# Performance work log

Measured on AMD Instinct MI355X. Metric: run time of the kernel, lower is better.

The kernel has to match this reference:

```python
import jax, jax.numpy as jnp
import numpy as np

N_NODES = 50000
N_EDGES = 800000
D_IN = 128
D_OUT = 128


def setup_inputs() -> dict:
    key = jax.random.key(0)
    k_feat, k_src, k_dst, k_ws, k_bs, k_wn = jax.random.split(key, 6)
    feat = jax.random.normal(k_feat, (N_NODES, D_IN), dtype=jnp.float32)
    src = jax.random.randint(k_src, (N_EDGES,), 0, N_NODES, dtype=jnp.int64)
    dst = jax.random.randint(k_dst, (N_EDGES,), 0, N_NODES, dtype=jnp.int64)
    # fc_self: Linear(D_IN, D_OUT, bias=True); fc_neigh: Linear(D_IN, D_OUT, bias=False)
    W_self = jax.random.normal(k_ws, (D_OUT, D_IN), dtype=jnp.float32) * (1.0 / np.sqrt(D_IN))
    b_self = jax.random.normal(k_bs, (D_OUT,), dtype=jnp.float32) * 0.01
    # xavier_uniform with relu gain
    gain = float(np.sqrt(2.0))
    bound = gain * float(np.sqrt(6.0 / (D_IN + D_OUT)))
    W_neigh = jax.random.uniform(k_wn, (D_OUT, D_IN), dtype=jnp.float32, minval=-bound, maxval=bound)
    bias = jnp.zeros((D_OUT,), dtype=jnp.float32)
    return {"feat": feat, "src": src, "dst": dst, "W_self": W_self,
            "b_self": b_self, "W_neigh": W_neigh, "bias": bias}


def reference(feat, src, dst, W_self, b_self, W_neigh, bias):
    # copy_u('h','m') + fn.mean('m','neigh'): gather src feats, mean-reduce by dst.
    # lin_before_mp is False (in_feats == out_feats), so aggregate raw feats first.
    n = feat.shape[0]
    msgs = feat[src]                                             # [E, D_IN]
    neigh_sum = jax.ops.segment_sum(msgs, dst, num_segments=n)   # [N, D_IN]
    deg = jax.ops.segment_sum(jnp.ones(src.shape, feat.dtype), dst, num_segments=n)
    # DGL mean yields 0 for zero-in-degree nodes
    h_neigh = jnp.where(deg[:, None] > 0, neigh_sum / jnp.maximum(deg, 1.0)[:, None], 0.0)
    h_neigh = h_neigh @ W_neigh.T                                # fc_neigh (no bias)
    h_self = feat @ W_self.T + b_self                            # fc_self
    return h_self + h_neigh + bias
```

## Files before the change

### kernel.cpp

```cpp
#include <hip/hip_runtime.h>
#include <hip/hip_fp8.h>

#define N_NODES 50000
#define N_EDGES 800000
#define D 128
#define NBUK 782
#define CAPB 1344
#define SRTN (CAPB + 64*7)
#define EPB 2048
#define SCAT_BLOCKS 391
#define FEAT_BLOCKS 3125
#define W_BLOCKS 32
#define CAPC 16

typedef __bf16 bf16x8 __attribute__((ext_vector_type(8)));
typedef __bf16 bf16x4 __attribute__((ext_vector_type(4)));
typedef float  f32x4  __attribute__((ext_vector_type(4)));
typedef float  f32x2  __attribute__((ext_vector_type(2)));

#if defined(__has_builtin)
#if __has_builtin(__builtin_amdgcn_cvt_pk_f32_fp8) && __has_builtin(__builtin_amdgcn_cvt_pk_fp8_f32)
#define HW_FP8 1
#endif
#endif

#define OFF_PACKED 0ull
#define OFF_FEAT8  19568768ull
#define OFF_WC16   25968896ull
#define OFF_BIASC  26034432ull
#define OFF_FEAT16 26035200ull

__device__ __forceinline__ float fp8tof_sw(unsigned char b) {
    __hip_fp8_e4m3 t; t.__x = b;
    return (float)t;
}

__global__ __launch_bounds__(256)
void prep_kernel(const int* __restrict__ src, const int* __restrict__ dst,
                 int* __restrict__ packed,
                 const float* __restrict__ feat, unsigned char* __restrict__ feat8,
                 __bf16* __restrict__ feat16,
                 const float* __restrict__ Ws, const float* __restrict__ Wn,
                 const float* __restrict__ b_self, const float* __restrict__ bias,
                 __bf16* __restrict__ Wc16, float* __restrict__ biasc, int n) {
    const int tid = threadIdx.x;
    const int bid = blockIdx.x;
    if (bid < SCAT_BLOCKS) {
        __shared__ int hist[NBUK];
        __shared__ int boff[NBUK];
        __shared__ int srtL[EPB];
        __shared__ int wtot[4];
        const int e0 = bid * EPB;
        int d[8], s[8];
        for (int i = tid; i < NBUK; i += 256) hist[i] = 0;
        __syncthreads();
        #pragma unroll
        for (int j = 0; j < 8; ++j) {
            int e = e0 + j * 256 + tid;
            bool ok = e < n;
            d[j] = ok ? dst[e] : -1;
            s[j] = ok ? src[e] : 0;
            if (ok) atomicAdd(&hist[d[j] >> 6], 1);
        }
        __syncthreads();
        {
            const int lane = tid & 63;
            const int wv = tid >> 6;
            const int b4 = tid * 4;
            int h0 = (b4 + 0 < NBUK) ? hist[b4 + 0] : 0;
            int h1 = (b4 + 1 < NBUK) ? hist[b4 + 1] : 0;
            int h2 = (b4 + 2 < NBUK) ? hist[b4 + 2] : 0;
            int h3 = (b4 + 3 < NBUK) ? hist[b4 + 3] : 0;
            int sm = h0 + h1 + h2 + h3;
            int v = sm;
            #pragma unroll
            for (int o = 1; o < 64; o <<= 1) {
                int u = __shfl_up(v, o);
                if (lane >= o) v += u;
            }
            if (lane == 63) wtot[wv] = v;
            __syncthreads();
            if (tid == 0) {
                int r = 0;
                #pragma unroll
                for (int j = 0; j < 4; ++j) { int t = wtot[j]; wtot[j] = r; r += t; }
            }
            __syncthreads();
            int ex = wtot[wv] + v - sm;
            if (b4 + 0 < NBUK) { boff[b4 + 0] = ex;                hist[b4 + 0] = 0; }
            if (b4 + 1 < NBUK) { boff[b4 + 1] = ex + h0;           hist[b4 + 1] = 0; }
            if (b4 + 2 < NBUK) { boff[b4 + 2] = ex + h0 + h1;      hist[b4 + 2] = 0; }
            if (b4 + 3 < NBUK) { boff[b4 + 3] = ex + h0 + h1 + h2; hist[b4 + 3] = 0; }
        }
        __syncthreads();
        #pragma unroll
        for (int j = 0; j < 8; ++j) {
            if (d[j] >= 0) {
                int bk = d[j] >> 6;
                int r = atomicAdd(&hist[bk], 1);
                srtL[boff[bk] + r] = ((d[j] & 63) << 16) | s[j];
            }
        }
        __syncthreads();
        for (int idx = tid; idx < NBUK * 4; idx += 256) {
            int bk = idx >> 2;
            int q4 = (idx & 3) * 4;
            int off = boff[bk];
            int c = hist[bk];
            int4 v;
            v.x = (q4 + 0 < c) ? srtL[off + q4 + 0] : -1;
            v.y = (q4 + 1 < c) ? srtL[off + q4 + 1] : -1;
            v.z = (q4 + 2 < c) ? srtL[off + q4 + 2] : -1;
            v.w = (q4 + 3 < c) ? srtL[off + q4 + 3] : -1;
            *(int4*)&packed[((size_t)bk * SCAT_BLOCKS + bid) * CAPC + q4] = v;
        }
    } else if (bid < SCAT_BLOCKS + FEAT_BLOCKS) {
        size_t i = ((size_t)(bid - SCAT_BLOCKS) * 256 + tid) * 8;
        float4 f0 = *(const float4*)(feat + i);
        float4 f1 = *(const float4*)(feat + i + 4);
        bf16x8 t16;
        t16[0]=(__bf16)f0.x; t16[1]=(__bf16)f0.y; t16[2]=(__bf16)f0.z; t16[3]=(__bf16)f0.w;
        t16[4]=(__bf16)f1.x; t16[5]=(__bf16)f1.y; t16[6]=(__bf16)f1.z; t16[7]=(__bf16)f1.w;
        *(bf16x8*)(feat16 + i) = t16;
#ifdef HW_FP8
        int q0 = __builtin_amdgcn_cvt_pk_fp8_f32(f0.x, f0.y, 0, false);
        q0     = __builtin_amdgcn_cvt_pk_fp8_f32(f0.z, f0.w, q0, true);
        int q1 = __builtin_amdgcn_cvt_pk_fp8_f32(f1.x, f1.y, 0, false);
        q1     = __builtin_amdgcn_cvt_pk_fp8_f32(f1.z, f1.w, q1, true);
        uint2 qq; qq.x = (unsigned)q0; qq.y = (unsigned)q1;
        *(uint2*)(feat8 + i) = qq;
#else
        float fv[8] = {f0.x, f0.y, f0.z, f0.w, f1.x, f1.y, f1.z, f1.w};
        union { unsigned char b[8]; unsigned long long u; } q;
        #pragma unroll
        for (int j = 0; j < 8; ++j) { __hip_fp8_e4m3 e(fv[j]); q.b[j] = e.__x; }
        *(unsigned long long*)(feat8 + i) = q.u;
#endif
    } else if (bid < SCAT_BLOCKS + FEAT_BLOCKS + W_BLOCKS) {
        int idx = (bid - SCAT_BLOCKS - FEAT_BLOCKS) * 256 + tid;
        int col = idx >> 6;
        int kq  = (idx & 63) * 4;
        const float* srcp = (kq < D) ? (Ws + (size_t)col * D + kq)
                                     : (Wn + (size_t)col * D + (kq - D));
        float4 f = *(const float4*)srcp;
        bf16x4 t;
        t[0]=(__bf16)f.x; t[1]=(__bf16)f.y; t[2]=(__bf16)f.z; t[3]=(__bf16)f.w;
        *(bf16x4*)(Wc16 + (size_t)col * 256 + kq) = t;
    } else {
        if (tid < D) biasc[tid] = b_self[tid] + bias[tid];
        else if (tid < D + 32)
            ((unsigned*)(feat8 + (size_t)N_NODES * D))[tid - 128] = 0u;
    }
}

__global__ __launch_bounds__(512)
void fused_kernel(const __bf16* __restrict__ feat16,
                  const unsigned char* __restrict__ feat8,
                  const int* __restrict__ packed,
                  const __bf16* __restrict__ Wc16,
                  const float* __restrict__ biasc,
                  float* __restrict__ out) {
    __shared__ __bf16 At[64][264];
    __shared__ unsigned short srt[SRTN];
    __shared__ int cnt[64];
    __shared__ int loff[64];
    __shared__ int degs[64];
    const int tid = threadIdx.x;
    const int b = blockIdx.x;
    const int node0 = b * 64;

    const int srow = tid >> 3;
    const int scol = (tid & 7) * 16;
    const int snn = node0 + srow;
    bf16x8 st0 = {}, st1 = {};
    if (snn < N_NODES) {
        const __bf16* sp = feat16 + (size_t)snn * D + scol;
        st0 = *(const bf16x8*)sp;
        st1 = *(const bf16x8*)(sp + 8);
    }

    if (tid < 64) cnt[tid] = 0;
    __syncthreads();

    int4 vv0, vv1, vv2, vv3;
    {
        const int4* sp = (const int4*)(packed + (size_t)b * SCAT_BLOCKS * CAPC);
        int4 none; none.x = -1; none.y = -1; none.z = -1; none.w = -1;
        int i0 = tid, i1 = 512 + tid, i2 = 1024 + tid, i3 = 1536 + tid;
        vv0 = sp[i0];
        vv1 = sp[i1];
        vv2 = (i2 < SCAT_BLOCKS * 4) ? sp[i2] : none;
        vv3 = (i3 < SCAT_BLOCKS * 4) ? sp[i3] : none;
        #define HISTV(v) do { \
            if ((v).x != -1) atomicAdd(&cnt[(v).x >> 16], 1); \
            if ((v).y != -1) atomicAdd(&cnt[(v).y >> 16], 1); \
            if ((v).z != -1) atomicAdd(&cnt[(v).z >> 16], 1); \
            if ((v).w != -1) atomicAdd(&cnt[(v).w >> 16], 1); } while (0)
        HISTV(vv0); HISTV(vv1); HISTV(vv2); HISTV(vv3);
        #undef HISTV
    }
    __syncthreads();

    if (tid < 64) {
        int c = cnt[tid];
        int cp = (c + 7) & ~7;
        int v = cp;
        #pragma unroll
        for (int o = 1; o < 64; o <<= 1) {
            int u = __shfl_up(v, o);
            if (tid >= o) v += u;
        }
        loff[tid] = v - cp;
        degs[tid] = c;
        cnt[tid] = 0;
    }
    __syncthreads();

    *(bf16x8*)&At[srow][scol] = st0;
    *(bf16x8*)&At[srow][scol + 8] = st1;
    {
        #define SCATV(v) do { \
            if ((v).x != -1) { int l = (v).x >> 16; int r = atomicAdd(&cnt[l], 1); int o = loff[l] + r; if (o < SRTN) srt[o] = (unsigned short)(v).x; } \
            if ((v).y != -1) { int l = (v).y >> 16; int r = atomicAdd(&cnt[l], 1); int o = loff[l] + r; if (o < SRTN) srt[o] = (unsigned short)(v).y; } \
            if ((v).z != -1) { int l = (v).z >> 16; int r = atomicAdd(&cnt[l], 1); int o = loff[l] + r; if (o < SRTN) srt[o] = (unsigned short)(v).z; } \
            if ((v).w != -1) { int l = (v).w >> 16; int r = atomicAdd(&cnt[l], 1); int o = loff[l] + r; if (o < SRTN) srt[o] = (unsigned short)(v).w; } } while (0)
        SCATV(vv0); SCATV(vv1); SCATV(vv2); SCATV(vv3);
        #undef SCATV
    }
    if (tid < 64) {
        int c = degs[tid];
        int cp = (c + 7) & ~7;
        int base0 = loff[tid];
        for (int j = c; j < cp; ++j)
            if (base0 + j < SRTN) srt[base0 + j] = (unsigned short)N_NODES;
    }
    __syncthreads();

    {
        const int hw = tid >> 5;
        const int lane = tid & 31;
        const unsigned int* g8 = (const unsigned int*)feat8;
        #pragma unroll
        for (int t = 0; t < 4; ++t) {
            int i = hw + t * 16;
            int dg = degs[i];
            int dgp = (dg + 7) & ~7;
            const int base0 = loff[i];
            float a0 = 0.f, a1 = 0.f, a2 = 0.f, a3 = 0.f;
            for (int j = 0; j < dgp; j += 8) {
                int s[8]; unsigned int w[8];
                #pragma unroll
                for (int q = 0; q < 8; ++q) s[q] = srt[base0 + j + q];
                #pragma unroll
                for (int q = 0; q < 8; ++q)
                    w[q] = g8[(size_t)s[q] * 32 + lane];
                #pragma unroll
                for (int q = 0; q < 8; ++q) {
#ifdef HW_FP8
                    f32x2 lo = __builtin_amdgcn_cvt_pk_f32_fp8((int)w[q], false);
                    f32x2 hi = __builtin_amdgcn_cvt_pk_f32_fp8((int)w[q], true);
                    a0 += lo[0]; a1 += lo[1]; a2 += hi[0]; a3 += hi[1];
#else
                    a0 += fp8tof_sw(w[q] & 0xFF);
                    a1 += fp8tof_sw((w[q] >> 8) & 0xFF);
                    a2 += fp8tof_sw((w[q] >> 16) & 0xFF);
                    a3 += fp8tof_sw(w[q] >> 24);
#endif
                }
            }
            float sc = dg > 0 ? 1.0f / (float)dg : 0.f;
            bf16x4 hv;
            hv[0] = (__bf16)(a0 * sc); hv[1] = (__bf16)(a1 * sc);
            hv[2] = (__bf16)(a2 * sc); hv[3] = (__bf16)(a3 * sc);
            *(bf16x4*)&At[i][128 + lane * 4] = hv;
        }
    }
    __syncthreads();

    const int wv = tid >> 6;
    const int lane = tid & 63;
    const int m = lane & 15;
    const int quad = lane >> 4;
    const int r0 = (wv & 1) * 32;
    const int c0 = (wv >> 1) * 32;

    f32x4 acc[2][2] = {};
    #pragma unroll
    for (int k0 = 0; k0 < 256; k0 += 32) {
        const int kk = k0 + quad * 8;
        bf16x8 a0 = *(const bf16x8*)&At[r0 + m][kk];
        bf16x8 a1 = *(const bf16x8*)&At[r0 + 16 + m][kk];
        #pragma unroll
        for (int ct = 0; ct < 2; ++ct) {
            int col = c0 + ct * 16 + m;
            bf16x8 bb = *(const bf16x8*)(Wc16 + (size_t)col * 256 + kk);
            acc[0][ct] = __builtin_amdgcn_mfma_f32_16x16x32_bf16(a0, bb, acc[0][ct], 0, 0, 0);
            acc[1][ct] = __builtin_amdgcn_mfma_f32_16x16x32_bf16(a1, bb, acc[1][ct], 0, 0, 0);
        }
    }

    #pragma unroll
    for (int ct = 0; ct < 2; ++ct) {
        int col = c0 + ct * 16 + m;
        float bb = biasc[col];
        #pragma unroll
        for (int rt = 0; rt < 2; ++rt) {
            int rowb = node0 + r0 + rt * 16 + quad * 4;
            #pragma unroll
            for (int r = 0; r < 4; ++r) {
                int nn = rowb + r;
                if (nn < N_NODES)
                    out[(size_t)nn * D + col] = acc[rt][ct][r] + bb;
            }
        }
    }
}

extern "C" void kernel_launch(void* const* d_in, const int* in_sizes, int n_in,
                              void* d_out, int out_size, void* d_ws, size_t ws_size,
                              hipStream_t stream) {
    const float* feat    = (const float*)d_in[0];
    const int*   src     = (const int*)d_in[1];
    const int*   dst     = (const int*)d_in[2];
    const float* W_self  = (const float*)d_in[3];
    const float* b_self  = (const float*)d_in[4];
    const float* W_neigh = (const float*)d_in[5];
    const float* bias    = (const float*)d_in[6];
    float* out = (float*)d_out;
    char*  ws  = (char*)d_ws;

    int* packed  = (int*)(ws + OFF_PACKED);
    unsigned char* feat8 = (unsigned char*)(ws + OFF_FEAT8);
    __bf16* Wc16   = (__bf16*)(ws + OFF_WC16);
    float*  biasc  = (float*)(ws + OFF_BIASC);
    __bf16* feat16 = (__bf16*)(ws + OFF_FEAT16);
    const int n_edges = in_sizes[1];

    prep_kernel<<<dim3(SCAT_BLOCKS + FEAT_BLOCKS + W_BLOCKS + 1), 256, 0, stream>>>(
        src, dst, packed, feat, feat8, feat16, W_self, W_neigh, b_self, bias,
        Wc16, biasc, n_edges);
    fused_kernel<<<dim3(NBUK), 512, 0, stream>>>(
        feat16, feat8, packed, Wc16, biasc, out);
}
```

Before: 129.0 us.

## Split each bucket across two 32-node blocks and drop bf16 feature copy

The fused kernel now launches twice as many 256-thread blocks, each handling half of a 64-node bucket. Each block filters the bucket's packed edges by half and builds a smaller local sort buffer. The prep kernel no longer writes a bf16 copy of the features; the fused kernel instead reads fp32 features directly and converts them when loading its self rows. This is meant to raise occupancy and cut a large global write and read, at the cost of each block scanning the full packed bucket list and re-reading it twice.

```diff
diff --git a/kernel.cpp b/kernel.cpp
--- a/kernel.cpp
+++ b/kernel.cpp
@@ -5,13 +5,12 @@
 #define N_EDGES 800000
 #define D 128
 #define NBUK 782
-#define CAPB 1344
-#define SRTN (CAPB + 64*7)
 #define EPB 2048
 #define SCAT_BLOCKS 391
 #define FEAT_BLOCKS 3125
 #define W_BLOCKS 32
 #define CAPC 16
+#define SRTN2 1024
 
 typedef __bf16 bf16x8 __attribute__((ext_vector_type(8)));
 typedef __bf16 bf16x4 __attribute__((ext_vector_type(4)));
@@ -28,7 +27,6 @@
 #define OFF_FEAT8  19568768ull
 #define OFF_WC16   25968896ull
 #define OFF_BIASC  26034432ull
-#define OFF_FEAT16 26035200ull
 
 __device__ __forceinline__ float fp8tof_sw(unsigned char b) {
     __hip_fp8_e4m3 t; t.__x = b;
@@ -39,7 +37,6 @@
 void prep_kernel(const int* __restrict__ src, const int* __restrict__ dst,
                  int* __restrict__ packed,
                  const float* __restrict__ feat, unsigned char* __restrict__ feat8,
-                 __bf16* __restrict__ feat16,
                  const float* __restrict__ Ws, const float* __restrict__ Wn,
                  const float* __restrict__ b_self, const float* __restrict__ bias,
                  __bf16* __restrict__ Wc16, float* __restrict__ biasc, int n) {
@@ -118,10 +115,6 @@
         size_t i = ((size_t)(bid - SCAT_BLOCKS) * 256 + tid) * 8;
         float4 f0 = *(const float4*)(feat + i);
         float4 f1 = *(const float4*)(feat + i + 4);
-        bf16x8 t16;
-        t16[0]=(__bf16)f0.x; t16[1]=(__bf16)f0.y; t16[2]=(__bf16)f0.z; t16[3]=(__bf16)f0.w;
-        t16[4]=(__bf16)f1.x; t16[5]=(__bf16)f1.y; t16[6]=(__bf16)f1.z; t16[7]=(__bf16)f1.w;
-        *(bf16x8*)(feat16 + i) = t16;
 #ifdef HW_FP8
         int q0 = __builtin_amdgcn_cvt_pk_fp8_f32(f0.x, f0.y, 0, false);
         q0     = __builtin_amdgcn_cvt_pk_fp8_f32(f0.z, f0.w, q0, true);
@@ -153,60 +146,60 @@
     }
 }
 
-__global__ __launch_bounds__(512)
-void fused_kernel(const __bf16* __restrict__ feat16,
+__global__ __launch_bounds__(256)
+void fused_kernel(const float* __restrict__ feat,
                   const unsigned char* __restrict__ feat8,
                   const int* __restrict__ packed,
                   const __bf16* __restrict__ Wc16,
                   const float* __restrict__ biasc,
                   float* __restrict__ out) {
-    __shared__ __bf16 At[64][264];
-    __shared__ unsigned short srt[SRTN];
-    __shared__ int cnt[64];
-    __shared__ int loff[64];
-    __shared__ int degs[64];
+    __shared__ __bf16 At[32][264];
+    __shared__ unsigned short srt[SRTN2];
+    __shared__ int cnt[32];
+    __shared__ int loff[32];
+    __shared__ int degs[32];
     const int tid = threadIdx.x;
-    const int b = blockIdx.x;
-    const int node0 = b * 64;
+    const int bid = blockIdx.x;
+    const int buk = bid >> 1;
+    const int half = bid & 1;
+    const int node0 = bid * 32;
 
     const int srow = tid >> 3;
     const int scol = (tid & 7) * 16;
     const int snn = node0 + srow;
     bf16x8 st0 = {}, st1 = {};
     if (snn < N_NODES) {
-        const __bf16* sp = feat16 + (size_t)snn * D + scol;
-        st0 = *(const bf16x8*)sp;
-        st1 = *(const bf16x8*)(sp + 8);
-    }
-
-    if (tid < 64) cnt[tid] = 0;
-    __syncthreads();
-
-    int4 vv0, vv1, vv2, vv3;
-    {
-        const int4* sp = (const int4*)(packed + (size_t)b * SCAT_BLOCKS * CAPC);
-        int4 none; none.x = -1; none.y = -1; none.z = -1; none.w = -1;
-        int i0 = tid, i1 = 512 + tid, i2 = 1024 + tid, i3 = 1536 + tid;
-        vv0 = sp[i0];
-        vv1 = sp[i1];
-        vv2 = (i2 < SCAT_BLOCKS * 4) ? sp[i2] : none;
-        vv3 = (i3 < SCAT_BLOCKS * 4) ? sp[i3] : none;
-        #define HISTV(v) do { \
-            if ((v).x != -1) atomicAdd(&cnt[(v).x >> 16], 1); \
-            if ((v).y != -1) atomicAdd(&cnt[(v).y >> 16], 1); \
-            if ((v).z != -1) atomicAdd(&cnt[(v).z >> 16], 1); \
-            if ((v).w != -1) atomicAdd(&cnt[(v).w >> 16], 1); } while (0)
-        HISTV(vv0); HISTV(vv1); HISTV(vv2); HISTV(vv3);
-        #undef HISTV
-    }
-    __syncthreads();
-
-    if (tid < 64) {
+        const float* fp = feat + (size_t)snn * D + scol;
+        float4 f0 = *(const float4*)(fp);
+        float4 f1 = *(const float4*)(fp + 4);
+        float4 f2 = *(const float4*)(fp + 8);
+        float4 f3 = *(const float4*)(fp + 12);
+        st0[0]=(__bf16)f0.x; st0[1]=(__bf16)f0.y; st0[2]=(__bf16)f0.z; st0[3]=(__bf16)f0.w;
+        st0[4]=(__bf16)f1.x; st0[5]=(__bf16)f1.y; st0[6]=(__bf16)f1.z; st0[7]=(__bf16)f1.w;
+        st1[0]=(__bf16)f2.x; st1[1]=(__bf16)f2.y; st1[2]=(__bf16)f2.z; st1[3]=(__bf16)f2.w;
+        st1[4]=(__bf16)f3.x; st1[5]=(__bf16)f3.y; st1[6]=(__bf16)f3.z; st1[7]=(__bf16)f3.w;
+    }
+
+    if (tid < 32) cnt[tid] = 0;
+    __syncthreads();
+
+    const int4* sp = (const int4*)(packed + (size_t)buk * SCAT_BLOCKS * CAPC);
+
+    #define HISTC(x) do { if ((x) != -1) { int l_ = (x) >> 16; \
+        if ((l_ >> 5) == half) atomicAdd(&cnt[l_ & 31], 1); } } while (0)
+    for (int i = tid; i < SCAT_BLOCKS * 4; i += 256) {
+        int4 v = sp[i];
+        HISTC(v.x); HISTC(v.y); HISTC(v.z); HISTC(v.w);
+    }
+    #undef HISTC
+    __syncthreads();
+
+    if (tid < 32) {
         int c = cnt[tid];
         int cp = (c + 7) & ~7;
         int v = cp;
         #pragma unroll
-        for (int o = 1; o < 64; o <<= 1) {
+        for (int o = 1; o < 32; o <<= 1) {
             int u = __shfl_up(v, o);
             if (tid >= o) v += u;
         }
@@ -218,21 +211,21 @@
 
     *(bf16x8*)&At[srow][scol] = st0;
     *(bf16x8*)&At[srow][scol + 8] = st1;
-    {
-        #define SCATV(v) do { \
-            if ((v).x != -1) { int l = (v).x >> 16; int r = atomicAdd(&cnt[l], 1); int o = loff[l] + r; if (o < SRTN) srt[o] = (unsigned short)(v).x; } \
-            if ((v).y != -1) { int l = (v).y >> 16; int r = atomicAdd(&cnt[l], 1); int o = loff[l] + r; if (o < SRTN) srt[o] = (unsigned short)(v).y; } \
-            if ((v).z != -1) { int l = (v).z >> 16; int r = atomicAdd(&cnt[l], 1); int o = loff[l] + r; if (o < SRTN) srt[o] = (unsigned short)(v).z; } \
-            if ((v).w != -1) { int l = (v).w >> 16; int r = atomicAdd(&cnt[l], 1); int o = loff[l] + r; if (o < SRTN) srt[o] = (unsigned short)(v).w; } } while (0)
-        SCATV(vv0); SCATV(vv1); SCATV(vv2); SCATV(vv3);
-        #undef SCATV
-    }
-    if (tid < 64) {
+    #define SCATC(x) do { if ((x) != -1) { int l_ = (x) >> 16; \
+        if ((l_ >> 5) == half) { int ll_ = l_ & 31; \
+            int r_ = atomicAdd(&cnt[ll_], 1); int o_ = loff[ll_] + r_; \
+            if (o_ < SRTN2) srt[o_] = (unsigned short)(x); } } } while (0)
+    for (int i = tid; i < SCAT_BLOCKS * 4; i += 256) {
+        int4 v = sp[i];
+        SCATC(v.x); SCATC(v.y); SCATC(v.z); SCATC(v.w);
+    }
+    #undef SCATC
+    if (tid < 32) {
         int c = degs[tid];
         int cp = (c + 7) & ~7;
         int base0 = loff[tid];
         for (int j = c; j < cp; ++j)
-            if (base0 + j < SRTN) srt[base0 + j] = (unsigned short)N_NODES;
+            if (base0 + j < SRTN2) srt[base0 + j] = (unsigned short)N_NODES;
     }
     __syncthreads();
 
@@ -242,7 +235,7 @@
         const unsigned int* g8 = (const unsigned int*)feat8;
         #pragma unroll
         for (int t = 0; t < 4; ++t) {
-            int i = hw + t * 16;
+            int i = hw + t * 8;
             int dg = degs[i];
             int dgp = (dg + 7) & ~7;
             const int base0 = loff[i];
@@ -281,15 +274,14 @@
     const int lane = tid & 63;
     const int m = lane & 15;
     const int quad = lane >> 4;
-    const int r0 = (wv & 1) * 32;
-    const int c0 = (wv >> 1) * 32;
+    const int c0 = wv * 32;
 
     f32x4 acc[2][2] = {};
     #pragma unroll
     for (int k0 = 0; k0 < 256; k0 += 32) {
         const int kk = k0 + quad * 8;
-        bf16x8 a0 = *(const bf16x8*)&At[r0 + m][kk];
-        bf16x8 a1 = *(const bf16x8*)&At[r0 + 16 + m][kk];
+        bf16x8 a0 = *(const bf16x8*)&At[m][kk];
+        bf16x8 a1 = *(const bf16x8*)&At[16 + m][kk];
         #pragma unroll
         for (int ct = 0; ct < 2; ++ct) {
             int col = c0 + ct * 16 + m;
@@ -305,7 +297,7 @@
         float bb = biasc[col];
         #pragma unroll
         for (int rt = 0; rt < 2; ++rt) {
-            int rowb = node0 + r0 + rt * 16 + quad * 4;
+            int rowb = node0 + rt * 16 + quad * 4;
             #pragma unroll
             for (int r = 0; r < 4; ++r) {
                 int nn = rowb + r;
@@ -331,14 +323,13 @@
 
     int* packed  = (int*)(ws + OFF_PACKED);
     unsigned char* feat8 = (unsigned char*)(ws + OFF_FEAT8);
-    __bf16* Wc16   = (__bf16*)(ws + OFF_WC16);
-    float*  biasc  = (float*)(ws + OFF_BIASC);
-    __bf16* feat16 = (__bf16*)(ws + OFF_FEAT16);
+    __bf16* Wc16  = (__bf16*)(ws + OFF_WC16);
+    float*  biasc = (float*)(ws + OFF_BIASC);
     const int n_edges = in_sizes[1];
 
     prep_kernel<<<dim3(SCAT_BLOCKS + FEAT_BLOCKS + W_BLOCKS + 1), 256, 0, stream>>>(
-        src, dst, packed, feat, feat8, feat16, W_self, W_neigh, b_self, bias,
+        src, dst, packed, feat, feat8, W_self, W_neigh, b_self, bias,
         Wc16, biasc, n_edges);
-    fused_kernel<<<dim3(NBUK), 512, 0, stream>>>(
-        feat16, feat8, packed, Wc16, biasc, out);
+    fused_kernel<<<dim3(NBUK * 2), 256, 0, stream>>>(
+        feat, feat8, packed, Wc16, biasc, out);
 }
```

Measured after the change: 134.2 us. 1.04x slower.
